# Performance work log

Measured on AMD Instinct MI355X. Metric: run time of the kernel, lower is better.

## Reference

```python
import jax, jax.numpy as jnp
import numpy as np

K_MAX = 64      # config.k_max
N_HASH = 8      # LSH hash bits per table


def setup_inputs() -> dict:
    key = jax.random.key(0)
    kq, kk, kw = jax.random.split(key, 3)
    B, L, D = 4, 2048, 64
    query = jax.random.normal(kq, (B, L, D), dtype=jnp.float32)
    key_t = jax.random.normal(kk, (B, L, D), dtype=jnp.float32)
    W = jax.random.normal(kw, (D, N_HASH), dtype=jnp.float32)  # LSH projection
    return {"query": query, "key": key_t, "W": W, "head_idx": 0}


def _hash_code(x, W):
    # binary_quantize then LSH hash: sign bits of random projection, packed to one int code
    x_bin = jnp.where(x > 0, 1.0, 0.0)                      # [B,L,D]
    bits = (jnp.einsum('bld,dh->blh', x_bin, W) > 0)        # [B,L,H] bool
    weights = (2 ** jnp.arange(N_HASH, dtype=jnp.int32))    # pack bits -> bucket id
    return jnp.sum(bits.astype(jnp.int32) * weights, axis=-1)  # [B,L] int32


def reference(query, key, W, head_idx):
    B, L, _ = query.shape
    q_code = _hash_code(query, W)   # [B,L]
    k_code = _hash_code(key, W)     # [B,L]
    # hash-equality match matrix [B, Lq, Lk] (== .all(dim=2) on hash bits)
    matches = q_code[:, :, None] == k_code[:, None, :]
    idx = jnp.arange(L, dtype=jnp.int32)
    # non-matches get sentinel L so the k_max smallest indices are the first matches
    cand_keys = jnp.where(matches, idx[None, None, :], L)   # [B,L,L]
    neg_top, _ = jax.lax.top_k(-cand_keys, K_MAX)           # k_max smallest indices
    cand = -neg_top                                          # ascending first-match order
    return jnp.where(cand == L, -1, cand).astype(jnp.int64)  # [B,L,k_max], -1 padded
```

## Files before the change

### kernel.cpp

```cpp
#include <hip/hip_runtime.h>

#define D 64
#define H 8
#define LSEQ 2048
#define KMAX 64
#define NCODES 256

__global__ void code_kernel(const float* __restrict__ query,
                            const float* __restrict__ key,
                            const float* __restrict__ W,
                            int* __restrict__ q_code,
                            int* __restrict__ k_code,
                            int n_pos) {
    __shared__ float Ws[D * H];
    for (int i = threadIdx.x; i < D * H; i += blockDim.x) Ws[i] = W[i];
    __syncthreads();

    int t = blockIdx.x * blockDim.x + threadIdx.x;
    if (t >= 2 * n_pos) return;

    const float* xp = (t < n_pos) ? (query + (size_t)t * D)
                                  : (key + (size_t)(t - n_pos) * D);
    float s[H];
#pragma unroll
    for (int h = 0; h < H; ++h) s[h] = 0.0f;

    for (int d4 = 0; d4 < D / 4; ++d4) {
        float4 xv = ((const float4*)xp)[d4];
        const float* x4 = (const float*)&xv;
#pragma unroll
        for (int k = 0; k < 4; ++k) {
            if (x4[k] > 0.0f) {
                int d = d4 * 4 + k;
#pragma unroll
                for (int h = 0; h < H; ++h) s[h] += Ws[d * H + h];
            }
        }
    }
    int c = 0;
#pragma unroll
    for (int h = 0; h < H; ++h) c |= (s[h] > 0.0f) ? (1 << h) : 0;

    if (t < n_pos) q_code[t] = c;
    else           k_code[t - n_pos] = c;
}

__global__ void __launch_bounds__(64)
bucket_ballot_kernel(const int* __restrict__ k_code,
                     int* __restrict__ bucket,
                     int* __restrict__ cnt) {
    int c = blockIdx.x & (NCODES - 1);
    int b = blockIdx.x >> 8;
    int lane = threadIdx.x;

    const int* kc = k_code + (size_t)b * LSEQ;
    int* bkt = bucket + ((size_t)b * NCODES + c) * KMAX;

    unsigned long long lt_mask = (lane == 63) ? 0x7FFFFFFFFFFFFFFFull
                                              : ((1ull << lane) - 1ull);
    int base = 0;
#pragma unroll 4
    for (int i = 0; i < LSEQ / 64; ++i) {
        int idx = i * 64 + lane;
        int ci = kc[idx];
        unsigned long long mask = __ballot(ci == c);
        if (ci == c) {
            int rank = base + __popcll(mask & lt_mask);
            if (rank < KMAX) bkt[rank] = idx;
        }
        base += __popcll(mask);
        if (base >= KMAX) break;
    }
    if (lane == 0) cnt[b * NCODES + c] = (base < KMAX) ? base : KMAX;
}

__global__ void emit_kernel(const int* __restrict__ q_code,
                            const int* __restrict__ bucket,
                            const int* __restrict__ cnt,
                            int* __restrict__ out, int total) {
    int t = blockIdx.x * blockDim.x + threadIdx.x;
    if (t >= total) return;
    int q = t >> 6;
    int j = t & (KMAX - 1);
    int b = q >> 11;
    int c = q_code[q];
    int row = b * NCODES + c;
    int n = cnt[row];
    out[t] = (j < n) ? bucket[(size_t)row * KMAX + j] : -1;
}

extern "C" void kernel_launch(void* const* d_in, const int* in_sizes, int n_in,
                              void* d_out, int out_size, void* d_ws, size_t ws_size,
                              hipStream_t stream) {
    const float* query = (const float*)d_in[0];
    const float* key   = (const float*)d_in[1];
    const float* W     = (const float*)d_in[2];

    int n_pos = in_sizes[0] / D;
    int B     = n_pos / LSEQ;

    int* q_code = (int*)d_ws;
    int* k_code = q_code + n_pos;
    int* bucket = k_code + n_pos;
    int* cnt    = bucket + (size_t)B * NCODES * KMAX;

    {
        int threads = 256;
        int blocks = (2 * n_pos + threads - 1) / threads;
        code_kernel<<<blocks, threads, 0, stream>>>(query, key, W,
                                                    q_code, k_code, n_pos);
    }
    {
        bucket_ballot_kernel<<<B * NCODES, 64, 0, stream>>>(k_code, bucket, cnt);
    }
    {
        int total = out_size;
        int threads = 256;
        int blocks = (total + threads - 1) / threads;
        emit_kernel<<<blocks, threads, 0, stream>>>(q_code, bucket, cnt,
                                                    (int*)d_out, total);
    }
}
```

Measured before the change: 81.37 us.

## Fuse bucket build and output emission into one per-code kernel

Merges the bucket-building and emit kernels. Each (batch, code) block keeps its first-match list in shared memory, then scans the query codes and writes that row for every matching query. This removes one launch and the global bucket/count round trip. Code kernel blocks also shrink to 64 threads. In exchange, each block scans all 2048 query codes, and output writes are scattered rows that each block issues serially per matching query, so load balance depends on the code distribution.

After: 89.01 us. 1.09x slower.

```diff
diff --git a/kernel.cpp b/kernel.cpp
--- a/kernel.cpp
+++ b/kernel.cpp
@@ -6,12 +6,13 @@
 #define KMAX 64
 #define NCODES 256
 
-__global__ void code_kernel(const float* __restrict__ query,
-                            const float* __restrict__ key,
-                            const float* __restrict__ W,
-                            int* __restrict__ q_code,
-                            int* __restrict__ k_code,
-                            int n_pos) {
+__global__ void __launch_bounds__(64)
+code_kernel(const float* __restrict__ query,
+            const float* __restrict__ key,
+            const float* __restrict__ W,
+            int* __restrict__ q_code,
+            int* __restrict__ k_code,
+            int n_pos) {
     __shared__ float Ws[D * H];
     for (int i = threadIdx.x; i < D * H; i += blockDim.x) Ws[i] = W[i];
     __syncthreads();
@@ -46,47 +47,47 @@
 }
 
 __global__ void __launch_bounds__(64)
-bucket_ballot_kernel(const int* __restrict__ k_code,
-                     int* __restrict__ bucket,
-                     int* __restrict__ cnt) {
+bucket_emit_kernel(const int* __restrict__ q_code,
+                   const int* __restrict__ k_code,
+                   int* __restrict__ out) {
+    __shared__ int row[KMAX];
     int c = blockIdx.x & (NCODES - 1);
     int b = blockIdx.x >> 8;
     int lane = threadIdx.x;
 
     const int* kc = k_code + (size_t)b * LSEQ;
-    int* bkt = bucket + ((size_t)b * NCODES + c) * KMAX;
+    const int* qc = q_code + (size_t)b * LSEQ;
+
+    row[lane] = -1;
+    __syncthreads();
 
     unsigned long long lt_mask = (lane == 63) ? 0x7FFFFFFFFFFFFFFFull
                                               : ((1ull << lane) - 1ull);
     int base = 0;
-#pragma unroll 4
     for (int i = 0; i < LSEQ / 64; ++i) {
         int idx = i * 64 + lane;
         int ci = kc[idx];
         unsigned long long mask = __ballot(ci == c);
         if (ci == c) {
             int rank = base + __popcll(mask & lt_mask);
-            if (rank < KMAX) bkt[rank] = idx;
+            if (rank < KMAX) row[rank] = idx;
         }
         base += __popcll(mask);
         if (base >= KMAX) break;
     }
-    if (lane == 0) cnt[b * NCODES + c] = (base < KMAX) ? base : KMAX;
-}
+    __syncthreads();
+    int myval = row[lane];
 
-__global__ void emit_kernel(const int* __restrict__ q_code,
-                            const int* __restrict__ bucket,
-                            const int* __restrict__ cnt,
-                            int* __restrict__ out, int total) {
-    int t = blockIdx.x * blockDim.x + threadIdx.x;
-    if (t >= total) return;
-    int q = t >> 6;
-    int j = t & (KMAX - 1);
-    int b = q >> 11;
-    int c = q_code[q];
-    int row = b * NCODES + c;
-    int n = cnt[row];
-    out[t] = (j < n) ? bucket[(size_t)row * KMAX + j] : -1;
+    for (int i = 0; i < LSEQ / 64; ++i) {
+        int qi = i * 64 + lane;
+        unsigned long long qmask = __ballot(qc[qi] == c);
+        while (qmask) {
+            int bit = (int)__ffsll((long long)qmask) - 1;
+            int q = i * 64 + bit;
+            out[((size_t)b * LSEQ + q) * KMAX + lane] = myval;
+            qmask &= qmask - 1;
+        }
+    }
 }
 
 extern "C" void kernel_launch(void* const* d_in, const int* in_sizes, int n_in,
@@ -101,23 +102,14 @@
 
     int* q_code = (int*)d_ws;
     int* k_code = q_code + n_pos;
-    int* bucket = k_code + n_pos;
-    int* cnt    = bucket + (size_t)B * NCODES * KMAX;
 
     {
-        int threads = 256;
-        int blocks = (2 * n_pos + threads - 1) / threads;
-        code_kernel<<<blocks, threads, 0, stream>>>(query, key, W,
-                                                    q_code, k_code, n_pos);
+        int total = 2 * n_pos;
+        code_kernel<<<(total + 63) / 64, 64, 0, stream>>>(query, key, W,
+                                                          q_code, k_code, n_pos);
     }
     {
-        bucket_ballot_kernel<<<B * NCODES, 64, 0, stream>>>(k_code, bucket, cnt);
-    }
-    {
-        int total = out_size;
-        int threads = 256;
-        int blocks = (total + threads - 1) / threads;
-        emit_kernel<<<blocks, threads, 0, stream>>>(q_code, bucket, cnt,
-                                                    (int*)d_out, total);
+        bucket_emit_kernel<<<B * NCODES, 64, 0, stream>>>(q_code, k_code,
+                                                          (int*)d_out);
     }
 }
```
